# Performance work log

Measured on AMD Instinct MI355X. Metric: run time of the kernel, lower is better.

Reference implementation:

```python
import jax, jax.numpy as jnp
import numpy as np
from jax import lax

B, L, DIN, H = 16, 100, 6144, 1024
DI, N, DTR, K, NC = 2048, 16, 64, 4, 16  # d_inner, d_state, dt_rank, d_conv, num_classes


def setup_inputs() -> dict:
    key = jax.random.key(0)
    ks = jax.random.split(key, 10)
    def s(k, shape, sc=0.02):
        return jax.random.normal(k, shape, dtype=jnp.float32) * sc
    return dict(
        x=jax.random.normal(ks[0], (B, L, DIN), dtype=jnp.float32),
        W_in=s(ks[1], (DIN, H)), b_in=jnp.zeros((H,), jnp.float32),
        in_proj_w=s(ks[2], (H, 2 * DI)),
        conv_w=s(ks[3], (DI, K), 0.1), conv_b=jnp.zeros((DI,), jnp.float32),
        x_proj_w=s(ks[4], (DI, DTR + 2 * N)),
        dt_proj_w=s(ks[5], (DTR, DI), 0.1),
        dt_proj_b=jnp.full((DI,), float(np.log(np.expm1(0.01))), jnp.float32),
        A_log=jnp.log(jnp.broadcast_to(jnp.arange(1, N + 1, dtype=jnp.float32), (DI, N))),
        D=jnp.ones((DI,), jnp.float32),
        out_proj_w=s(ks[6], (DI, H)),
        W_out=s(ks[7], (H, NC)), b_out=jnp.zeros((NC,), jnp.float32),
    )


def reference(x, W_in, b_in, in_proj_w, conv_w, conv_b, x_proj_w,
              dt_proj_w, dt_proj_b, A_log, D, out_proj_w, W_out, b_out):
    # input projection: [B,L,DIN] -> [B,L,H]
    h = x @ W_in + b_in
    # Mamba block
    xz = h @ in_proj_w                      # [B,L,2*DI]
    xm, z = xz[..., :DI], xz[..., DI:]
    # depthwise causal conv1d, kernel K
    xp = jnp.pad(xm, ((0, 0), (K - 1, 0), (0, 0)))
    xc = sum(conv_w[:, k] * xp[:, k:k + L, :] for k in range(K)) + conv_b
    xc = jax.nn.silu(xc)                    # [B,L,DI]
    # input-dependent dt, B, C
    proj = xc @ x_proj_w                    # [B,L,DTR+2N]
    dt = proj[..., :DTR]
    Bm = proj[..., DTR:DTR + N]             # [B,L,N]
    Cm = proj[..., DTR + N:]                # [B,L,N]
    delta = jax.nn.softplus(dt @ dt_proj_w + dt_proj_b)  # [B,L,DI]
    A = -jnp.exp(A_log)                     # [DI,N]
    dA = jnp.exp(jnp.einsum('bld,dn->bldn', delta, A))          # [B,L,DI,N]
    dBx = (delta * xc)[..., None] * Bm[:, :, None, :]            # [B,L,DI,N]
    # selective scan over time: h_t = dA_t * h_{t-1} + dBx_t
    def step(hprev, inp):
        dA_t, dBx_t = inp
        hnew = dA_t * hprev + dBx_t
        return hnew, hnew
    h0 = jnp.zeros((xm.shape[0], DI, N), xm.dtype)
    _, hs = lax.scan(step, h0, (dA.transpose(1, 0, 2, 3), dBx.transpose(1, 0, 2, 3)))
    y = jnp.einsum('lbdn,bln->bld', hs, Cm)  # [B,L,DI]
    y = y + D * xc
    y = y * jax.nn.silu(z)
    out = y @ out_proj_w                     # [B,L,H]
    logits = out @ W_out + b_out             # [B,L,NC]
    return logits
```

## Files before the change

### kernel.cpp

```cpp
#include <hip/hip_runtime.h>
#include <hip/hip_bf16.h>
#include <stdint.h>

constexpr int Bb  = 16;
constexpr int Ll  = 100;
constexpr int DIN = 6144;
constexpr int Hh  = 1024;
constexpr int DI  = 2048;
constexpr int Nst = 16;
constexpr int DTR = 64;
constexpr int Kc  = 4;
constexpr int NC  = 16;
constexpr int M   = Bb * Ll;
constexpr int NCH = 4;
constexpr int CL  = Ll / NCH;

typedef __attribute__((ext_vector_type(8))) short short8;
typedef __attribute__((ext_vector_type(4))) float floatx4;

__device__ __forceinline__ float bf2f(unsigned short u) {
    union { uint32_t b; float f; } x; x.b = ((uint32_t)u) << 16; return x.f;
}
__device__ __forceinline__ unsigned short f2bf(float f) {
    union { float f; uint32_t b; } x; x.f = f;
    uint32_t r = x.b + 0x7FFF + ((x.b >> 16) & 1);
    return (unsigned short)(r >> 16);
}
__device__ __forceinline__ float fast_silu(float x) {
    return x / (1.f + __expf(-x));
}

__global__ __launch_bounds__(256) void prep_kernel(
    const float* __restrict__ x, unsigned short* __restrict__ x_bf,
    const float* __restrict__ W_in, unsigned short* __restrict__ Wt_in,
    const float* __restrict__ W_ip, unsigned short* __restrict__ Wt_ip,
    const float* __restrict__ W_op, unsigned short* __restrict__ Wt_op,
    const float* __restrict__ xpw,  unsigned short* __restrict__ xpw_t,
    const float* __restrict__ dtw,  unsigned short* __restrict__ dtw_t)
{
    __shared__ float t[32][33];
    int b = blockIdx.x;

    if (b < 9600) {
        int i = (b * 256 + threadIdx.x) * 4;
        float4 v = *(const float4*)&x[i];
        x_bf[i + 0] = f2bf(v.x);
        x_bf[i + 1] = f2bf(v.y);
        x_bf[i + 2] = f2bf(v.z);
        x_bf[i + 3] = f2bf(v.w);
        return;
    }
    const float* in; unsigned short* out; int K, N, bid;
    if      (b < 15744) { in = W_in; out = Wt_in; K = DIN; N = Hh;     bid = b - 9600;  }
    else if (b < 19840) { in = W_ip; out = Wt_ip; K = Hh;  N = 2 * DI; bid = b - 15744; }
    else if (b < 21888) { in = W_op; out = Wt_op; K = DI;  N = Hh;     bid = b - 19840; }
    else if (b < 22080) { in = xpw;  out = xpw_t; K = DI;  N = 96;     bid = b - 21888; }
    else                { in = dtw;  out = dtw_t; K = DTR; N = DI;     bid = b - 22080; }

    int kx = bid % (K / 32), ny = bid / (K / 32);
    int k0 = kx * 32, n0 = ny * 32;
    int tx = threadIdx.x & 31, ty = threadIdx.x >> 5;
    #pragma unroll
    for (int i = 0; i < 4; i++)
        t[ty + i * 8][tx] = in[(size_t)(k0 + ty + i * 8) * N + n0 + tx];
    __syncthreads();
    #pragma unroll
    for (int i = 0; i < 4; i++)
        out[(size_t)(n0 + ty + i * 8) * K + k0 + tx] = f2bf(t[tx][ty + i * 8]);
}

template<bool SPLIT, bool BIAS, bool W16>
__global__ __launch_bounds__(512) void gemm_deep(
    const unsigned short* __restrict__ A, int lda,
    const unsigned short* __restrict__ Bt, int ldb,
    const float* __restrict__ bias,
    unsigned short* __restrict__ C16,
    unsigned short* __restrict__ Cpart,
    int Md, int Nd, int Kslab)
{
    __shared__ short As[3 * 256 * 64];
    __shared__ short Bs[3 * 128 * 64];

    const int nx = gridDim.x, ny = gridDim.y, nz = gridDim.z;
    const int nb = nx * ny * nz;
    int id = blockIdx.x + nx * (blockIdx.y + ny * blockIdx.z);
    int bx, by, bz;
    if ((nb & 7) == 0) {
        int swz = (id & 7) * (nb >> 3) + (id >> 3);
        bx = swz % nx;
        int rem = swz / nx;
        by = rem % ny;
        bz = rem / ny;
    } else {
        bx = blockIdx.x; by = blockIdx.y; bz = blockIdx.z;
    }

    const int tid  = threadIdx.x;
    const int lane = tid & 63;
    const int wid  = tid >> 6;
    const int wr   = wid >> 1;
    const int wc   = wid & 1;
    const int l15  = lane & 15;
    const int kg   = lane >> 4;
    const int gsw  = l15 & 7;
    const int m0   = bx * 256;
    const int n0   = by * 128;
    const int kbeg = SPLIT ? bz * Kslab : 0;

    floatx4 acc[4][4];
    #pragma unroll
    for (int m = 0; m < 4; m++)
        #pragma unroll
        for (int n = 0; n < 4; n++)
            acc[m][n] = (floatx4){0.f, 0.f, 0.f, 0.f};

    auto stage = [&](int buf, int k0) {
        #pragma unroll
        for (int j = 0; j < 4; j++) {
            int c = j * 512 + tid;
            int row = c >> 3, gl = c & 7;
            int gg = gl ^ (row & 7);
            int grow = m0 + row; grow = grow < Md ? grow : Md - 1;
            const __attribute__((address_space(1))) short* src =
                (const __attribute__((address_space(1))) short*)(A + (size_t)grow * lda + k0 + gg * 8);
            __builtin_amdgcn_global_load_lds(
                (const __attribute__((address_space(1))) void*)src,
                (__attribute__((address_space(3))) void*)&As[(buf * 2048 + c) * 8], 16, 0, 0);
        }
        #pragma unroll
        for (int j = 0; j < 2; j++) {
            int c = j * 512 + tid;
            int row = c >> 3, gl = c & 7;
            int gg = gl ^ (row & 7);
            int brow = n0 + row; brow = brow < Nd ? brow : Nd - 1;
            const __attribute__((address_space(1))) short* src =
                (const __attribute__((address_space(1))) short*)(Bt + (size_t)brow * ldb + k0 + gg * 8);
            __builtin_amdgcn_global_load_lds(
                (const __attribute__((address_space(1))) void*)src,
                (__attribute__((address_space(3))) void*)&Bs[(buf * 1024 + c) * 8], 16, 0, 0);
        }
    };

    const int nt = Kslab >> 6;
    stage(0, kbeg);
    stage(1, kbeg + 64);

    for (int t = 0; t < nt; t++) {
        const int cur = t % 3;
        if (t + 2 < nt) {
            stage((t + 2) % 3, kbeg + (t + 2) * 64);
            asm volatile("s_waitcnt vmcnt(12)" ::: "memory");
        } else if (t + 1 < nt) {
            asm volatile("s_waitcnt vmcnt(6)" ::: "memory");
        } else {
            asm volatile("s_waitcnt vmcnt(0)" ::: "memory");
        }
        __builtin_amdgcn_s_barrier();
        __builtin_amdgcn_sched_barrier(0);

        short8 a[2][4], bfr[2][4];
        #pragma unroll
        for (int kk = 0; kk < 2; kk++) {
            #pragma unroll
            for (int m = 0; m < 4; m++) {
                int row = wr * 64 + m * 16 + l15;
                int gs  = (kk * 4 + kg) ^ gsw;
                a[kk][m] = *(const short8*)&As[(cur * 2048 + row * 8 + gs) * 8];
            }
            #pragma unroll
            for (int n = 0; n < 4; n++) {
                int row = wc * 64 + n * 16 + l15;
                int gs  = (kk * 4 + kg) ^ gsw;
                bfr[kk][n] = *(const short8*)&Bs[(cur * 1024 + row * 8 + gs) * 8];
            }
        }
        asm volatile("s_waitcnt lgkmcnt(0)" ::: "memory");
        __builtin_amdgcn_sched_barrier(0);
        __builtin_amdgcn_s_barrier();
        __builtin_amdgcn_sched_barrier(0);

        __builtin_amdgcn_s_setprio(1);
        #pragma unroll
        for (int kk = 0; kk < 2; kk++)
            #pragma unroll
            for (int m = 0; m < 4; m++)
                #pragma unroll
                for (int n = 0; n < 4; n++)
                    acc[m][n] = __builtin_amdgcn_mfma_f32_16x16x32_bf16(a[kk][m], bfr[kk][n], acc[m][n], 0, 0, 0);
        __builtin_amdgcn_s_setprio(0);
    }

    unsigned short* Cs = (unsigned short*)As;
    #pragma unroll
    for (int n = 0; n < 4; n++) {
        int col = wc * 64 + n * 16 + l15;
        float bv = BIAS ? bias[n0 + col] : 0.f;
        #pragma unroll
        for (int m = 0; m < 4; m++) {
            #pragma unroll
            for (int q = 0; q < 4; q++) {
                int row = wr * 64 + m * 16 + kg * 4 + q;
                Cs[row * 136 + col] = f2bf(acc[m][n][q] + bv);
            }
        }
    }
    __syncthreads();
    #pragma unroll
    for (int j = 0; j < 8; j++) {
        int c = j * 512 + tid;
        int row = c >> 4, cc = c & 15;
        int grow = m0 + row;
        if (grow >= Md) continue;
        short8 v = *(const short8*)&Cs[row * 136 + cc * 8];
        if (SPLIT)
            *(short8*)&Cpart[(size_t)bz * Md * Nd + (size_t)grow * Nd + n0 + cc * 8] = v;
        else if (W16)
            *(short8*)&C16[(size_t)grow * Nd + n0 + cc * 8] = v;
    }
}

template<bool SPLIT, bool PARTBF, bool BIAS, int ACT, bool W32, bool W16>
__global__ __launch_bounds__(256) void gemm_mfma(
    const unsigned short* __restrict__ A, int lda,
    const unsigned short* __restrict__ Bt, int ldb,
    const float* __restrict__ bias,
    float* __restrict__ C32,
    unsigned short* __restrict__ C16,
    void* __restrict__ Cpart,
    int Md, int Nd, int Kslab)
{
    __shared__ short As[2][128 * 64];
    __shared__ short Bs[2][128 * 64];

    const int nx = gridDim.x, ny = gridDim.y, nz = gridDim.z;
    const int nb = nx * ny * nz;
    int id = blockIdx.x + nx * (blockIdx.y + ny * blockIdx.z);
    int bx, by, bz;
    if ((nb & 7) == 0) {
        int swz = (id & 7) * (nb >> 3) + (id >> 3);
        bx = swz % nx;
        int rem = swz / nx;
        by = rem % ny;
        bz = rem / ny;
    } else {
        bx = blockIdx.x; by = blockIdx.y; bz = blockIdx.z;
    }

    const int tid  = threadIdx.x;
    const int lane = tid & 63;
    const int wid  = tid >> 6;
    const int wr   = wid >> 1;
    const int wc   = wid & 1;
    const int l15  = lane & 15;
    const int kg   = lane >> 4;
    const int gsw  = l15 & 7;
    const int m0   = bx * 128;
    const int n0   = by * 128;
    const int kbeg = SPLIT ? bz * Kslab : 0;

    floatx4 acc[4][4];
    #pragma unroll
    for (int m = 0; m < 4; m++)
        #pragma unroll
        for (int n = 0; n < 4; n++)
            acc[m][n] = (floatx4){0.f, 0.f, 0.f, 0.f};

    auto stage = [&](int buf, int k0) {
        #pragma unroll
        for (int j = 0; j < 4; j++) {
            int c = j * 256 + tid;
            int row = c >> 3, gl = c & 7;
            int gg = gl ^ (row & 7);
            int grow = m0 + row; grow = grow < Md ? grow : Md - 1;
            const __attribute__((address_space(1))) short* src =
                (const __attribute__((address_space(1))) short*)(A + (size_t)grow * lda + k0 + gg * 8);
            __builtin_amdgcn_global_load_lds(
                (const __attribute__((address_space(1))) void*)src,
                (__attribute__((address_space(3))) void*)&As[buf][c * 8], 16, 0, 0);
        }
        #pragma unroll
        for (int j = 0; j < 4; j++) {
            int c = j * 256 + tid;
            int row = c >> 3, gl = c & 7;
            int gg = gl ^ (row & 7);
            int brow = n0 + row; brow = brow < Nd ? brow : Nd - 1;
            const __attribute__((address_space(1))) short* src =
                (const __attribute__((address_space(1))) short*)(Bt + (size_t)brow * ldb + k0 + gg * 8);
            __builtin_amdgcn_global_load_lds(
                (const __attribute__((address_space(1))) void*)src,
                (__attribute__((address_space(3))) void*)&Bs[buf][c * 8], 16, 0, 0);
        }
    };

    stage(0, kbeg);
    asm volatile("s_waitcnt vmcnt(0)" ::: "memory");
    __builtin_amdgcn_s_barrier();
    __builtin_amdgcn_sched_barrier(0);

    const int nt = Kslab >> 6;
    for (int t = 0; t < nt; t++) {
        const int cur = t & 1;
        if (t + 1 < nt) {
            stage(cur ^ 1, kbeg + (t + 1) * 64);
            asm volatile("s_waitcnt vmcnt(8)" ::: "memory");
        } else {
            asm volatile("s_waitcnt vmcnt(0)" ::: "memory");
        }
        __builtin_amdgcn_s_barrier();
        __builtin_amdgcn_sched_barrier(0);

        short8 a[2][4], bfr[2][4];
        #pragma unroll
        for (int kk = 0; kk < 2; kk++) {
            #pragma unroll
            for (int m = 0; m < 4; m++) {
                int row = wr * 64 + m * 16 + l15;
                int gs  = (kk * 4 + kg) ^ gsw;
                a[kk][m] = *(const short8*)&As[cur][(row * 8 + gs) * 8];
            }
            #pragma unroll
            for (int n = 0; n < 4; n++) {
                int row = wc * 64 + n * 16 + l15;
                int gs  = (kk * 4 + kg) ^ gsw;
                bfr[kk][n] = *(const short8*)&Bs[cur][(row * 8 + gs) * 8];
            }
        }
        __builtin_amdgcn_s_setprio(1);
        #pragma unroll
        for (int kk = 0; kk < 2; kk++)
            #pragma unroll
            for (int m = 0; m < 4; m++)
                #pragma unroll
                for (int n = 0; n < 4; n++)
                    acc[m][n] = __builtin_amdgcn_mfma_f32_16x16x32_bf16(a[kk][m], bfr[kk][n], acc[m][n], 0, 0, 0);
        __builtin_amdgcn_s_setprio(0);
        __builtin_amdgcn_sched_barrier(0);
        __builtin_amdgcn_s_barrier();
    }

    if (SPLIT) {
        #pragma unroll
        for (int n = 0; n < 4; n++) {
            int col = n0 + wc * 64 + n * 16 + l15;
            if (col >= Nd) continue;
            #pragma unroll
            for (int m = 0; m < 4; m++)
                #pragma unroll
                for (int q = 0; q < 4; q++) {
                    int row = m0 + wr * 64 + m * 16 + kg * 4 + q;
                    if (row >= Md) continue;
                    size_t ix = (size_t)bz * Md * Nd + (size_t)row * Nd + col;
                    if (PARTBF) ((unsigned short*)Cpart)[ix] = f2bf(acc[m][n][q]);
                    else        ((float*)Cpart)[ix] = acc[m][n][q];
                }
        }
    } else {
        #pragma unroll
        for (int n = 0; n < 4; n++) {
            int col = n0 + wc * 64 + n * 16 + l15;
            if (col >= Nd) continue;
            float bv = BIAS ? bias[col] : 0.f;
            #pragma unroll
            for (int m = 0; m < 4; m++)
                #pragma unroll
                for (int q = 0; q < 4; q++) {
                    int row = m0 + wr * 64 + m * 16 + kg * 4 + q;
                    if (row >= Md) continue;
                    float v = acc[m][n][q] + bv;
                    if (ACT == 1) v = fmaxf(v, 0.f) + log1pf(expf(-fabsf(v)));
                    if (W32) C32[(size_t)row * Nd + col] = v;
                    if (W16) C16[(size_t)row * Nd + col] = f2bf(v);
                }
        }
    }
}

template<int S, bool BIAS, int ACT, bool W32, bool W16>
__global__ __launch_bounds__(256) void reduce_split(
    const float* __restrict__ P, const float* __restrict__ bias,
    float* __restrict__ C32, unsigned short* __restrict__ C16,
    int total, int nmask)
{
    int i = (blockIdx.x * 256 + threadIdx.x) * 4;
    float4 v = *(const float4*)&P[i];
    #pragma unroll
    for (int s = 1; s < S; s++) {
        float4 p = *(const float4*)&P[(size_t)s * total + i];
        v.x += p.x; v.y += p.y; v.z += p.z; v.w += p.w;
    }
    float r[4] = {v.x, v.y, v.z, v.w};
    #pragma unroll
    for (int j = 0; j < 4; j++) {
        float t = r[j];
        if (BIAS) t += bias[(i + j) & nmask];
        if (ACT == 1) t = fmaxf(t, 0.f) + log1pf(expf(-fabsf(t)));
        if (W32) C32[i + j] = t;
        if (W16) C16[i + j] = f2bf(t);
    }
}

template<int S, bool BIAS>
__global__ __launch_bounds__(256) void reduce_split_bf(
    const unsigned short* __restrict__ P, const float* __restrict__ bias,
    unsigned short* __restrict__ C16, int total, int nmask)
{
    int i = (blockIdx.x * 256 + threadIdx.x) * 8;
    float r[8] = {};
    #pragma unroll
    for (int s = 0; s < S; s++) {
        short8 p = *(const short8*)&P[(size_t)s * total + i];
        #pragma unroll
        for (int j = 0; j < 8; j++) r[j] += bf2f((unsigned short)p[j]);
    }
    short8 o;
    #pragma unroll
    for (int j = 0; j < 8; j++) {
        float t = r[j];
        if (BIAS) t += bias[(i + j) & nmask];
        o[j] = (short)f2bf(t);
    }
    *(short8*)&C16[i] = o;
}

__global__ __launch_bounds__(256) void conv_silu_kernel(
    const unsigned short* __restrict__ xz, const float* __restrict__ conv_w,
    const float* __restrict__ conv_b, float* __restrict__ xc,
    unsigned short* __restrict__ xc_bf)
{
    int idx = blockIdx.x * 256 + threadIdx.x;
    if (idx >= Bb * Ll * DI) return;
    int d  = idx & (DI - 1);
    int bl = idx >> 11;
    int l  = bl % Ll;

    float acc = conv_b[d];
    #pragma unroll
    for (int k = 0; k < Kc; k++) {
        int ls = l + k - (Kc - 1);
        if (ls >= 0)
            acc = fmaf(conv_w[d * Kc + k], bf2f(xz[(size_t)(bl + ls - l) * (2 * DI) + d]), acc);
    }
    float s = fast_silu(acc);
    xc[idx] = s;
    xc_bf[idx] = f2bf(s);
}

__global__ __launch_bounds__(256) void scan_part1(
    const float* __restrict__ delta, const float* __restrict__ xc,
    const float* __restrict__ proj,  const float* __restrict__ A_log,
    float* __restrict__ Pbuf, float* __restrict__ Sbuf)
{
    const int t    = threadIdx.x;
    const int nq   = t & 3;
    const int dloc = t >> 2;
    const int d    = blockIdx.x * 64 + dloc;
    const int b    = blockIdx.y;
    const int c    = blockIdx.z;

    float4 Alq = *(const float4*)&A_log[(size_t)d * Nst + nq * 4];
    float Ar0 = -expf(Alq.x), Ar1 = -expf(Alq.y), Ar2 = -expf(Alq.z), Ar3 = -expf(Alq.w);

    float h0 = 0.f, h1 = 0.f, h2 = 0.f, h3 = 0.f;
    float sdl = 0.f;

    for (int l = c * CL; l < (c + 1) * CL; l++) {
        size_t bl = (size_t)b * Ll + l;
        float dl  = delta[bl * DI + d];
        float xcv = xc[bl * DI + d];
        float dx  = dl * xcv;
        float4 Bv = *(const float4*)&proj[bl * (DTR + 2 * Nst) + DTR + nq * 4];

        h0 = fmaf(__expf(dl * Ar0), h0, dx * Bv.x);
        h1 = fmaf(__expf(dl * Ar1), h1, dx * Bv.y);
        h2 = fmaf(__expf(dl * Ar2), h2, dx * Bv.z);
        h3 = fmaf(__expf(dl * Ar3), h3, dx * Bv.w);
        sdl += dl;
    }

    size_t o = (((size_t)c * Bb + b) * DI + d) * Nst + nq * 4;
    *(float4*)&Pbuf[o] = (float4){__expf(sdl * Ar0), __expf(sdl * Ar1),
                                  __expf(sdl * Ar2), __expf(sdl * Ar3)};
    *(float4*)&Sbuf[o] = (float4){h0, h1, h2, h3};
}

__global__ __launch_bounds__(256) void scan_part2(
    const float* __restrict__ delta, const float* __restrict__ xc,
    const unsigned short* __restrict__ xz, const float* __restrict__ proj,
    const float* __restrict__ A_log, const float* __restrict__ Dv,
    const float* __restrict__ Pbuf, const float* __restrict__ Sbuf,
    unsigned short* __restrict__ y)
{
    const int t    = threadIdx.x;
    const int nq   = t & 3;
    const int dloc = t >> 2;
    const int d    = blockIdx.x * 64 + dloc;
    const int b    = blockIdx.y;
    const int c    = blockIdx.z;

    float4 Alq = *(const float4*)&A_log[(size_t)d * Nst + nq * 4];
    float Ar0 = -expf(Alq.x), Ar1 = -expf(Alq.y), Ar2 = -expf(Alq.z), Ar3 = -expf(Alq.w);
    const float Dd = Dv[d];

    float h0 = 0.f, h1 = 0.f, h2 = 0.f, h3 = 0.f;
    for (int cc = 0; cc < c; cc++) {
        size_t o = (((size_t)cc * Bb + b) * DI + d) * Nst + nq * 4;
        float4 Pv = *(const float4*)&Pbuf[o];
        float4 Sv = *(const float4*)&Sbuf[o];
        h0 = fmaf(Pv.x, h0, Sv.x);
        h1 = fmaf(Pv.y, h1, Sv.y);
        h2 = fmaf(Pv.z, h2, Sv.z);
        h3 = fmaf(Pv.w, h3, Sv.w);
    }

    for (int l = c * CL; l < (c + 1) * CL; l++) {
        size_t bl = (size_t)b * Ll + l;
        float dl  = delta[bl * DI + d];
        float xcv = xc[bl * DI + d];
        float zv  = bf2f(xz[bl * (2 * DI) + DI + d]);
        float dx  = dl * xcv;
        const float* p = proj + bl * (DTR + 2 * Nst);
        float4 Bv = *(const float4*)&p[DTR + nq * 4];
        float4 Cv = *(const float4*)&p[DTR + Nst + nq * 4];

        h0 = fmaf(__expf(dl * Ar0), h0, dx * Bv.x);
        h1 = fmaf(__expf(dl * Ar1), h1, dx * Bv.y);
        h2 = fmaf(__expf(dl * Ar2), h2, dx * Bv.z);
        h3 = fmaf(__expf(dl * Ar3), h3, dx * Bv.w);

        float yac = h0 * Cv.x + h1 * Cv.y + h2 * Cv.z + h3 * Cv.w;
        yac += __shfl_xor(yac, 1);
        yac += __shfl_xor(yac, 2);

        if (nq == 0) {
            float yv = yac + Dd * xcv;
            yv *= fast_silu(zv);
            y[bl * DI + d] = f2bf(yv);
        }
    }
}

__global__ __launch_bounds__(256) void gemm_n16(
    const unsigned short* __restrict__ A, const float* __restrict__ W,
    const float* __restrict__ bias, float* __restrict__ C, int Kd)
{
    int m  = blockIdx.x;
    int t  = threadIdx.x;
    int c  = t & 15;
    int kg = t >> 4;
    const unsigned short* a = A + (size_t)m * Kd;

    float acc = 0.f;
    for (int k = kg; k < Kd; k += 16)
        acc = fmaf(bf2f(a[k]), W[k * NC + c], acc);

    __shared__ float red[256];
    red[t] = acc;
    __syncthreads();
    #pragma unroll
    for (int s = 128; s >= 16; s >>= 1) {
        if (t < s) red[t] += red[t + s];
        __syncthreads();
    }
    if (t < 16) C[(size_t)m * NC + t] = red[t] + bias[t];
}

extern "C" void kernel_launch(void* const* d_in, const int* in_sizes, int n_in,
                              void* d_out, int out_size, void* d_ws, size_t ws_size,
                              hipStream_t stream) {
    const float* x         = (const float*)d_in[0];
    const float* W_in      = (const float*)d_in[1];
    const float* b_in      = (const float*)d_in[2];
    const float* in_proj_w = (const float*)d_in[3];
    const float* conv_w    = (const float*)d_in[4];
    const float* conv_b    = (const float*)d_in[5];
    const float* x_proj_w  = (const float*)d_in[6];
    const float* dt_proj_w = (const float*)d_in[7];
    const float* dt_proj_b = (const float*)d_in[8];
    const float* A_log     = (const float*)d_in[9];
    const float* Dv        = (const float*)d_in[10];
    const float* out_proj  = (const float*)d_in[11];
    const float* W_out     = (const float*)d_in[12];
    const float* b_out     = (const float*)d_in[13];
    float* logits = (float*)d_out;

    char* base = (char*)d_ws;
    size_t off = 0;
    auto alloc = [&](size_t bytes) {
        char* p = base + off;
        off += (bytes + 255) & ~(size_t)255;
        return p;
    };
    unsigned short* x_bf    = (unsigned short*)alloc((size_t)M * DIN * 2);
    unsigned short* Wt_in   = (unsigned short*)alloc((size_t)Hh * DIN * 2);
    unsigned short* Wt_ip   = (unsigned short*)alloc((size_t)(2 * DI) * Hh * 2);
    unsigned short* Wt_op   = (unsigned short*)alloc((size_t)Hh * DI * 2);
    unsigned short* xpw_t   = (unsigned short*)alloc((size_t)96 * DI * 2);
    unsigned short* dtw_t   = (unsigned short*)alloc((size_t)DI * DTR * 2);
    unsigned short* h_bf    = (unsigned short*)alloc((size_t)M * Hh * 2);
    unsigned short* xz_bf   = (unsigned short*)alloc((size_t)M * 2 * DI * 2);
    float*          xc      = (float*)alloc((size_t)M * DI * 4);
    float*          delta   = (float*)alloc((size_t)M * DI * 4);
    unsigned short* xc_bf   = (unsigned short*)alloc((size_t)M * DI * 2);
    float*          proj_f  = (float*)alloc((size_t)M * 96 * 4);
    unsigned short* proj_bf = (unsigned short*)alloc((size_t)M * 96 * 2);
    unsigned short* y_bf    = (unsigned short*)alloc((size_t)M * DI * 2);
    unsigned short* out_bf  = (unsigned short*)alloc((size_t)M * Hh * 2);

    unsigned short* P14 = (unsigned short*)xc;
    float*          P8  = delta;
    float*          Pbuf = (float*)x_bf;
    float*          Sbuf = Pbuf + (size_t)(NCH - 1) * Bb * DI * Nst;

    dim3 blk(256), blk5(512);

    prep_kernel<<<dim3(22208), blk, 0, stream>>>(
        x, x_bf, W_in, Wt_in, in_proj_w, Wt_ip, out_proj, Wt_op,
        x_proj_w, xpw_t, dt_proj_w, dtw_t);

    gemm_deep<true, false, false><<<dim3(7, Hh / 128, 4), blk5, 0, stream>>>(
        x_bf, DIN, Wt_in, DIN, nullptr, nullptr, P14, M, Hh, DIN / 4);
    reduce_split_bf<4, true><<<dim3((M * Hh) / 2048), blk, 0, stream>>>(
        P14, b_in, h_bf, M * Hh, Hh - 1);

    gemm_deep<false, false, true><<<dim3(7, (2 * DI) / 128, 1), blk5, 0, stream>>>(
        h_bf, Hh, Wt_ip, Hh, nullptr, xz_bf, nullptr, M, 2 * DI, Hh);

    conv_silu_kernel<<<dim3((Bb * Ll * DI) / 256), blk, 0, stream>>>(
        xz_bf, conv_w, conv_b, xc, xc_bf);

    gemm_mfma<true, false, false, 0, false, false><<<dim3(13, 1, 8), blk, 0, stream>>>(
        xc_bf, DI, xpw_t, DI, nullptr, nullptr, nullptr, P8, M, 96, DI / 8);
    reduce_split<8, false, 0, true, true><<<dim3((M * 96) / 1024), blk, 0, stream>>>(
        P8, nullptr, proj_f, proj_bf, M * 96, 0);

    gemm_mfma<false, false, true, 1, true, false><<<dim3(13, DI / 128, 1), blk, 0, stream>>>(
        proj_bf, 96, dtw_t, DTR, dt_proj_b, delta, nullptr, nullptr, M, DI, DTR);

    scan_part1<<<dim3(DI / 64, Bb, NCH - 1), blk, 0, stream>>>(
        delta, xc, proj_f, A_log, Pbuf, Sbuf);
    scan_part2<<<dim3(DI / 64, Bb, NCH), blk, 0, stream>>>(
        delta, xc, xz_bf, proj_f, A_log, Dv, Pbuf, Sbuf, y_bf);

    gemm_deep<true, false, false><<<dim3(7, Hh / 128, 4), blk5, 0, stream>>>(
        y_bf, DI, Wt_op, DI, nullptr, nullptr, P14, M, Hh, DI / 4);
    reduce_split_bf<4, false><<<dim3((M * Hh) / 2048), blk, 0, stream>>>(
        P14, nullptr, out_bf, M * Hh, 0);

    gemm_n16<<<dim3(M), blk, 0, stream>>>(out_bf, W_out, b_out, logits, Hh);
}
```

Measured before the change: 235.6 us.

## Split LDS fragment loads in gemm_deep, fuse chunk-0 scan output, drop reduce kernel

The deep GEMM inner loop now issues both halves of its LDS fragment loads, waits only on the first half, and runs the first half of the MFMAs while the second half is still in flight. scan_part1 now also writes y for chunk 0, since that chunk has no carried-in state, so scan_part2 launches one fewer chunk. The split-K reduce after the out_proj GEMM is removed and gemm_n16 sums the four bf16 partial slabs directly. That saves a launch and a write/read of an intermediate, but the small GEMM now reads four times as much data.

Measured after the change: 286.7 us. 1.22x slower.

```diff
diff --git a/kernel.cpp b/kernel.cpp
--- a/kernel.cpp
+++ b/kernel.cpp
@@ -160,20 +160,42 @@
 
         short8 a[2][4], bfr[2][4];
         #pragma unroll
-        for (int kk = 0; kk < 2; kk++) {
-            #pragma unroll
-            for (int m = 0; m < 4; m++) {
-                int row = wr * 64 + m * 16 + l15;
-                int gs  = (kk * 4 + kg) ^ gsw;
-                a[kk][m] = *(const short8*)&As[(cur * 2048 + row * 8 + gs) * 8];
-            }
-            #pragma unroll
-            for (int n = 0; n < 4; n++) {
-                int row = wc * 64 + n * 16 + l15;
-                int gs  = (kk * 4 + kg) ^ gsw;
-                bfr[kk][n] = *(const short8*)&Bs[(cur * 1024 + row * 8 + gs) * 8];
-            }
-        }
+        for (int m = 0; m < 4; m++) {
+            int row = wr * 64 + m * 16 + l15;
+            int gs  = kg ^ gsw;
+            a[0][m] = *(const short8*)&As[(cur * 2048 + row * 8 + gs) * 8];
+        }
+        #pragma unroll
+        for (int n = 0; n < 4; n++) {
+            int row = wc * 64 + n * 16 + l15;
+            int gs  = kg ^ gsw;
+            bfr[0][n] = *(const short8*)&Bs[(cur * 1024 + row * 8 + gs) * 8];
+        }
+        __builtin_amdgcn_sched_barrier(0);
+        #pragma unroll
+        for (int m = 0; m < 4; m++) {
+            int row = wr * 64 + m * 16 + l15;
+            int gs  = (4 + kg) ^ gsw;
+            a[1][m] = *(const short8*)&As[(cur * 2048 + row * 8 + gs) * 8];
+        }
+        #pragma unroll
+        for (int n = 0; n < 4; n++) {
+            int row = wc * 64 + n * 16 + l15;
+            int gs  = (4 + kg) ^ gsw;
+            bfr[1][n] = *(const short8*)&Bs[(cur * 1024 + row * 8 + gs) * 8];
+        }
+        __builtin_amdgcn_sched_barrier(0);
+        asm volatile("s_waitcnt lgkmcnt(8)" ::: "memory");
+        __builtin_amdgcn_sched_barrier(0);
+
+        __builtin_amdgcn_s_setprio(1);
+        #pragma unroll
+        for (int m = 0; m < 4; m++)
+            #pragma unroll
+            for (int n = 0; n < 4; n++)
+                acc[m][n] = __builtin_amdgcn_mfma_f32_16x16x32_bf16(a[0][m], bfr[0][n], acc[m][n], 0, 0, 0);
+        __builtin_amdgcn_s_setprio(0);
+        __builtin_amdgcn_sched_barrier(0);
         asm volatile("s_waitcnt lgkmcnt(0)" ::: "memory");
         __builtin_amdgcn_sched_barrier(0);
         __builtin_amdgcn_s_barrier();
@@ -181,12 +203,10 @@
 
         __builtin_amdgcn_s_setprio(1);
         #pragma unroll
-        for (int kk = 0; kk < 2; kk++)
-            #pragma unroll
-            for (int m = 0; m < 4; m++)
-                #pragma unroll
-                for (int n = 0; n < 4; n++)
-                    acc[m][n] = __builtin_amdgcn_mfma_f32_16x16x32_bf16(a[kk][m], bfr[kk][n], acc[m][n], 0, 0, 0);
+        for (int m = 0; m < 4; m++)
+            #pragma unroll
+            for (int n = 0; n < 4; n++)
+                acc[m][n] = __builtin_amdgcn_mfma_f32_16x16x32_bf16(a[1][m], bfr[1][n], acc[m][n], 0, 0, 0);
         __builtin_amdgcn_s_setprio(0);
     }
 
@@ -447,8 +467,10 @@
 
 __global__ __launch_bounds__(256) void scan_part1(
     const float* __restrict__ delta, const float* __restrict__ xc,
-    const float* __restrict__ proj,  const float* __restrict__ A_log,
-    float* __restrict__ Pbuf, float* __restrict__ Sbuf)
+    const unsigned short* __restrict__ xz, const float* __restrict__ proj,
+    const float* __restrict__ A_log, const float* __restrict__ Dv,
+    float* __restrict__ Pbuf, float* __restrict__ Sbuf,
+    unsigned short* __restrict__ y)
 {
     const int t    = threadIdx.x;
     const int nq   = t & 3;
@@ -456,9 +478,11 @@
     const int d    = blockIdx.x * 64 + dloc;
     const int b    = blockIdx.y;
     const int c    = blockIdx.z;
+    const bool emit = (c == 0);
 
     float4 Alq = *(const float4*)&A_log[(size_t)d * Nst + nq * 4];
     float Ar0 = -expf(Alq.x), Ar1 = -expf(Alq.y), Ar2 = -expf(Alq.z), Ar3 = -expf(Alq.w);
+    const float Dd = Dv[d];
 
     float h0 = 0.f, h1 = 0.f, h2 = 0.f, h3 = 0.f;
     float sdl = 0.f;
@@ -468,13 +492,27 @@
         float dl  = delta[bl * DI + d];
         float xcv = xc[bl * DI + d];
         float dx  = dl * xcv;
-        float4 Bv = *(const float4*)&proj[bl * (DTR + 2 * Nst) + DTR + nq * 4];
+        const float* p = proj + bl * (DTR + 2 * Nst);
+        float4 Bv = *(const float4*)&p[DTR + nq * 4];
 
         h0 = fmaf(__expf(dl * Ar0), h0, dx * Bv.x);
         h1 = fmaf(__expf(dl * Ar1), h1, dx * Bv.y);
         h2 = fmaf(__expf(dl * Ar2), h2, dx * Bv.z);
         h3 = fmaf(__expf(dl * Ar3), h3, dx * Bv.w);
         sdl += dl;
+
+        if (emit) {
+            float4 Cv = *(const float4*)&p[DTR + Nst + nq * 4];
+            float yac = h0 * Cv.x + h1 * Cv.y + h2 * Cv.z + h3 * Cv.w;
+            yac += __shfl_xor(yac, 1);
+            yac += __shfl_xor(yac, 2);
+            if (nq == 0) {
+                float zv = bf2f(xz[bl * (2 * DI) + DI + d]);
+                float yv = yac + Dd * xcv;
+                yv *= fast_silu(zv);
+                y[bl * DI + d] = f2bf(yv);
+            }
+        }
     }
 
     size_t o = (((size_t)c * Bb + b) * DI + d) * Nst + nq * 4;
@@ -495,7 +533,7 @@
     const int dloc = t >> 2;
     const int d    = blockIdx.x * 64 + dloc;
     const int b    = blockIdx.y;
-    const int c    = blockIdx.z;
+    const int c    = blockIdx.z + 1;
 
     float4 Alq = *(const float4*)&A_log[(size_t)d * Nst + nq * 4];
     float Ar0 = -expf(Alq.x), Ar1 = -expf(Alq.y), Ar2 = -expf(Alq.z), Ar3 = -expf(Alq.w);
@@ -540,18 +578,22 @@
 }
 
 __global__ __launch_bounds__(256) void gemm_n16(
-    const unsigned short* __restrict__ A, const float* __restrict__ W,
-    const float* __restrict__ bias, float* __restrict__ C, int Kd)
+    const unsigned short* __restrict__ P,
+    const float* __restrict__ W,
+    const float* __restrict__ bias, float* __restrict__ C, int Kd, int total)
 {
     int m  = blockIdx.x;
     int t  = threadIdx.x;
     int c  = t & 15;
     int kg = t >> 4;
-    const unsigned short* a = A + (size_t)m * Kd;
 
     float acc = 0.f;
-    for (int k = kg; k < Kd; k += 16)
-        acc = fmaf(bf2f(a[k]), W[k * NC + c], acc);
+    #pragma unroll
+    for (int s = 0; s < 4; s++) {
+        const unsigned short* a = P + (size_t)s * total + (size_t)m * Kd;
+        for (int k = kg; k < Kd; k += 16)
+            acc = fmaf(bf2f(a[k]), W[k * NC + c], acc);
+    }
 
     __shared__ float red[256];
     red[t] = acc;
@@ -604,7 +646,6 @@
     float*          proj_f  = (float*)alloc((size_t)M * 96 * 4);
     unsigned short* proj_bf = (unsigned short*)alloc((size_t)M * 96 * 2);
     unsigned short* y_bf    = (unsigned short*)alloc((size_t)M * DI * 2);
-    unsigned short* out_bf  = (unsigned short*)alloc((size_t)M * Hh * 2);
 
     unsigned short* P14 = (unsigned short*)xc;
     float*          P8  = delta;
@@ -637,14 +678,12 @@
         proj_bf, 96, dtw_t, DTR, dt_proj_b, delta, nullptr, nullptr, M, DI, DTR);
 
     scan_part1<<<dim3(DI / 64, Bb, NCH - 1), blk, 0, stream>>>(
-        delta, xc, proj_f, A_log, Pbuf, Sbuf);
-    scan_part2<<<dim3(DI / 64, Bb, NCH), blk, 0, stream>>>(
+        delta, xc, xz_bf, proj_f, A_log, Dv, Pbuf, Sbuf, y_bf);
+    scan_part2<<<dim3(DI / 64, Bb, NCH - 1), blk, 0, stream>>>(
         delta, xc, xz_bf, proj_f, A_log, Dv, Pbuf, Sbuf, y_bf);
 
     gemm_deep<true, false, false><<<dim3(7, Hh / 128, 4), blk5, 0, stream>>>(
         y_bf, DI, Wt_op, DI, nullptr, nullptr, P14, M, Hh, DI / 4);
-    reduce_split_bf<4, false><<<dim3((M * Hh) / 2048), blk, 0, stream>>>(
-        P14, nullptr, out_bf, M * Hh, 0);
-
-    gemm_n16<<<dim3(M), blk, 0, stream>>>(out_bf, W_out, b_out, logits, Hh);
-}
+
+    gemm_n16<<<dim3(M), blk, 0, stream>>>(P14, W_out, b_out, logits, Hh, M * Hh);
+}
```
